# Kernel optimization log

Hardware: AMD Instinct MI355X
Metric: run time of the kernel (lower is better)

## Reference

```python
import jax, jax.numpy as jnp
import numpy as np

N = 100000
E = 600000
HID = 128
L = 2
BN_EPS = 1e-5


def setup_inputs() -> dict:
    key = jax.random.key(0)
    ks = jax.random.split(key, 20)
    s = 0.05
    inp = {
        "x": jax.random.normal(ks[0], (N, 128), jnp.float32),
        "edge_index": jax.random.randint(ks[1], (2, E), 0, N, jnp.int64 if jax.config.jax_enable_x64 else jnp.int32),
        "edge_attr": jax.random.normal(ks[2], (E, 1), jnp.float32),
        # backbone params
        "lin_W": jax.random.normal(ks[3], (128, HID), jnp.float32) * s,
        "lin_b": jnp.zeros((HID,), jnp.float32),
        "enc_W": jax.random.normal(ks[4], (1, HID), jnp.float32) * s,
        "enc_b": jnp.zeros((HID,), jnp.float32),
        # per-layer GIN params, stacked over L layers
        "eps": jnp.zeros((L,), jnp.float32),
        "e1_W": jax.random.normal(ks[5], (L, 1, HID), jnp.float32) * s,
        "e1_b": jnp.zeros((L, HID), jnp.float32),
        "e2_W": jax.random.normal(ks[6], (L, HID, HID), jnp.float32) * s,
        "e2_b": jnp.zeros((L, HID), jnp.float32),
        "m1_W": jax.random.normal(ks[7], (L, HID, 2 * HID), jnp.float32) * s,
        "m1_b": jnp.zeros((L, 2 * HID), jnp.float32),
        "bn_g": jnp.ones((L, 2 * HID), jnp.float32),
        "bn_b": jnp.zeros((L, 2 * HID), jnp.float32),
        "m2_W": jax.random.normal(ks[8], (L, 2 * HID, HID), jnp.float32) * s,
        "m2_b": jnp.zeros((L, HID), jnp.float32),
    }
    return inp


def _gin_layer(h, src, dst, edge_attr, eps, e1_W, e1_b, e2_W, e2_b,
               m1_W, m1_b, bn_g, bn_b, m2_W, m2_b):
    # edge encoder: Linear(1,H) -> ReLU -> Linear(H,H)
    ee = jax.nn.relu(edge_attr @ e1_W + e1_b) @ e2_W + e2_b      # [E,H]
    msg = jax.nn.relu(h[src] + ee)                               # gather + relu
    agg = jax.ops.segment_sum(msg, dst, num_segments=h.shape[0])  # scatter-add
    z = (1.0 + eps) * h + agg
    z = z @ m1_W + m1_b                                          # [N,2H]
    mu = jnp.mean(z, axis=0)
    var = jnp.mean((z - mu) ** 2, axis=0)                        # biased (train-mode BN)
    z = (z - mu) * jax.lax.rsqrt(var + BN_EPS) * bn_g + bn_b
    z = jax.nn.relu(z)
    return z @ m2_W + m2_b                                       # [N,H]


def reference(x, edge_index, edge_attr, lin_W, lin_b, enc_W, enc_b, eps,
              e1_W, e1_b, e2_W, e2_b, m1_W, m1_b, bn_g, bn_b, m2_W, m2_b):
    src, dst = edge_index[0], edge_index[1]
    # in_dim > 1 -> linear projection path
    h = x @ lin_W + lin_b                                        # [N,H]
    ee0 = edge_attr @ enc_W + enc_b                              # [E,H]
    new_h = h.at[src].set(jax.nn.relu(h[src] + ee0))
    new_h = new_h.at[dst].set(jax.nn.relu(h[dst] + ee0))
    h = new_h
    for l in range(L):
        h = _gin_layer(h, src, dst, edge_attr, eps[l], e1_W[l], e1_b[l],
                       e2_W[l], e2_b[l], m1_W[l], m1_b[l], bn_g[l], bn_b[l],
                       m2_W[l], m2_b[l])
        if l < L - 1:
            h = jax.nn.relu(h)
        # dropout omitted for determinism
    return h
```

## Files before the change

kernel.cpp:

```cpp
#include <hip/hip_runtime.h>

#define N_NODES 100000
#define E_EDGES 600000
#define HID 128

typedef __attribute__((ext_vector_type(8))) short short8v;
typedef __attribute__((ext_vector_type(4))) float f32x4;

__device__ __forceinline__ unsigned short bf16rne(float x) {
  unsigned u = __float_as_uint(x);
  return (unsigned short)((u + 0x7FFFu + ((u >> 16) & 1u)) >> 16);
}
__device__ __forceinline__ float bf16tof(unsigned short u) {
  return __uint_as_float(((unsigned)u) << 16);
}

__global__ void k_last(const int* __restrict__ ei, int* __restrict__ last_src,
                       int* __restrict__ last_dst, int* __restrict__ deg, int E) {
  int e = blockIdx.x * blockDim.x + threadIdx.x;
  if (e >= E) return;
  int s = ei[e], d = ei[E + e];
  atomicMax(&last_src[s], e);
  atomicMax(&last_dst[d], e);
  atomicAdd(&deg[d], 1);
}

__global__ __launch_bounds__(256) void k_scan1(const int* __restrict__ deg,
                                               int* __restrict__ excl,
                                               int* __restrict__ bsum, int n) {
  __shared__ int sh[256];
  int b = blockIdx.x, t = threadIdx.x;
  int i0 = b * 1024 + t * 4;
  int v0 = (i0 + 0 < n) ? deg[i0 + 0] : 0;
  int v1 = (i0 + 1 < n) ? deg[i0 + 1] : 0;
  int v2 = (i0 + 2 < n) ? deg[i0 + 2] : 0;
  int v3 = (i0 + 3 < n) ? deg[i0 + 3] : 0;
  int tsum = v0 + v1 + v2 + v3;
  sh[t] = tsum;
  __syncthreads();
  for (int off = 1; off < 256; off <<= 1) {
    int add = (t >= off) ? sh[t - off] : 0;
    __syncthreads();
    sh[t] += add;
    __syncthreads();
  }
  int ex = sh[t] - tsum;
  if (i0 + 0 < n) excl[i0 + 0] = ex;
  if (i0 + 1 < n) excl[i0 + 1] = ex + v0;
  if (i0 + 2 < n) excl[i0 + 2] = ex + v0 + v1;
  if (i0 + 3 < n) excl[i0 + 3] = ex + v0 + v1 + v2;
  if (t == 255) bsum[b] = sh[255];
}

__global__ void k_scan2(const int* __restrict__ bsum, int* __restrict__ boff, int nb) {
  __shared__ int sh[128];
  int t = threadIdx.x;
  int v = (t < nb) ? bsum[t] : 0;
  sh[t] = v;
  __syncthreads();
  for (int off = 1; off < 128; off <<= 1) {
    int add = (t >= off) ? sh[t - off] : 0;
    __syncthreads();
    sh[t] += add;
    __syncthreads();
  }
  if (t < nb) boff[t] = sh[t] - v;
}

__global__ void k_scatter(const int* __restrict__ ei, const float* __restrict__ ea,
                          const int* __restrict__ excl, const int* __restrict__ boff,
                          int* __restrict__ cnt, int2* __restrict__ pairE, int E) {
  int e = blockIdx.x * blockDim.x + threadIdx.x;
  if (e >= E) return;
  int d = ei[E + e];
  int p = excl[d] + boff[d >> 10] + atomicAdd(&cnt[d], 1);
  pairE[p] = make_int2(ei[e], __float_as_int(ea[e]));
}

__global__ void k_table(const float* __restrict__ e1_W, const float* __restrict__ e1_b,
                        const float* __restrict__ e2_W, const float* __restrict__ e2_b,
                        float* __restrict__ tabA, float* __restrict__ tabB,
                        float* __restrict__ tsort) {
  const int l = blockIdx.x;
  const float* W1g = e1_W + l * 128;
  const float* b1g = e1_b + l * 128;
  const float* W2g = e2_W + l * 128 * 128;
  const float* b2g = e2_b + l * 128;
  float* tA = tabA + (size_t)l * 129 * 128;
  float* tB = tabB + (size_t)l * 129 * 128;
  float* tS = tsort + l * 128;
  __shared__ float w1[128], b1[128], key[128];
  __shared__ int idx[128];
  __shared__ float w2[128][128];
  const int t = threadIdx.x;
  w1[t] = W1g[t];
  b1[t] = b1g[t];
  for (int k = 0; k < 128; ++k) w2[k][t] = W2g[k * 128 + t];
  __syncthreads();
  float s0 = w1[t];
  key[t] = (s0 != 0.0f) ? (-b1[t] / s0) : __builtin_inff();
  idx[t] = t;
  for (int size = 2; size <= 128; size <<= 1) {
    for (int stride = size >> 1; stride > 0; stride >>= 1) {
      __syncthreads();
      int p = t ^ stride;
      if (p > t) {
        bool up = ((t & size) == 0);
        float k1 = key[t], k2 = key[p];
        if (up == (k1 > k2)) {
          int i1 = idx[t], i2 = idx[p];
          key[t] = k2; key[p] = k1; idx[t] = i2; idx[p] = i1;
        }
      }
    }
  }
  __syncthreads();
  tS[t] = key[t];
  float A = 0.0f, B = b2g[t];
  for (int k = 0; k < 128; ++k) {
    float s = w1[k], bb = b1[k], w = w2[k][t];
    if (s < 0.0f) { A = fmaf(s, w, A); B = fmaf(bb, w, B); }
    else if (s == 0.0f && bb > 0.0f) { B = fmaf(bb, w, B); }
  }
  tA[t] = A;
  tB[t] = B;
  for (int i = 0; i < 128; ++i) {
    float kv = key[i];
    int kk = idx[i];
    if (kv < __builtin_inff()) {
      float s = w1[kk], bb = b1[kk], w = w2[kk][t];
      if (s > 0.0f) { A = fmaf(s, w, A); B = fmaf(bb, w, B); }
      else { A = fmaf(-s, w, A); B = fmaf(-bb, w, B); }
    }
    tA[(i + 1) * 128 + t] = A;
    tB[(i + 1) * 128 + t] = B;
  }
}

__global__ __launch_bounds__(256) void k_pos(const int2* __restrict__ pairE,
                                             const float* __restrict__ tsort,
                                             unsigned char* __restrict__ posb0,
                                             unsigned char* __restrict__ posb1, int E) {
  __shared__ float ts0[128], ts1[128];
  if (threadIdx.x < 128) {
    ts0[threadIdx.x] = tsort[threadIdx.x];
    ts1[threadIdx.x] = tsort[128 + threadIdx.x];
  }
  __syncthreads();
  int i = blockIdx.x * blockDim.x + threadIdx.x;
  if (i >= E) return;
  float a = __int_as_float(pairE[i].y);
  int p0 = 0, p1 = 0;
#pragma unroll
  for (int st = 64; st > 0; st >>= 1) {
    if (p0 + st <= 128 && ts0[p0 + st - 1] < a) p0 += st;
    if (p1 + st <= 128 && ts1[p1 + st - 1] < a) p1 += st;
  }
  posb0[i] = (unsigned char)p0;
  posb1[i] = (unsigned char)p1;
}

__global__ __launch_bounds__(256) void k_agg(
    const unsigned short* __restrict__ h, const int2* __restrict__ pairE,
    const unsigned char* __restrict__ posb, const int* __restrict__ excl,
    const int* __restrict__ boff, const float* __restrict__ tabA,
    const float* __restrict__ tabB, const float* __restrict__ epsP,
    unsigned* __restrict__ zin, int N, int E) {
  int w = __builtin_amdgcn_readfirstlane((int)((blockIdx.x * 256 + threadIdx.x) >> 6));
  if (w >= N) return;
  int lane = threadIdx.x & 63;
  int start = excl[w] + boff[w >> 10];
  int end = (w + 1 < N) ? (excl[w + 1] + boff[(w + 1) >> 10]) : E;
  int j = lane * 2;
  float a0 = 0.0f, a1 = 0.0f, c0 = 0.0f, c1 = 0.0f;
  int i = start;
  for (; i + 2 <= end; i += 2) {
    int2 pr0 = pairE[i], pr1 = pairE[i + 1];
    int p0 = posb[i], p1 = posb[i + 1];
    float aa = __int_as_float(pr0.y), ab = __int_as_float(pr1.y);
    unsigned hv0 = *(const unsigned*)(h + (size_t)pr0.x * HID + j);
    float2 A0 = *(const float2*)(tabA + (size_t)p0 * HID + j);
    float2 B0 = *(const float2*)(tabB + (size_t)p0 * HID + j);
    unsigned hv1 = *(const unsigned*)(h + (size_t)pr1.x * HID + j);
    float2 A1 = *(const float2*)(tabA + (size_t)p1 * HID + j);
    float2 B1 = *(const float2*)(tabB + (size_t)p1 * HID + j);
    a0 += fmaxf(__uint_as_float(hv0 << 16) + fmaf(A0.x, aa, B0.x), 0.0f);
    a1 += fmaxf(__uint_as_float(hv0 & 0xFFFF0000u) + fmaf(A0.y, aa, B0.y), 0.0f);
    c0 += fmaxf(__uint_as_float(hv1 << 16) + fmaf(A1.x, ab, B1.x), 0.0f);
    c1 += fmaxf(__uint_as_float(hv1 & 0xFFFF0000u) + fmaf(A1.y, ab, B1.y), 0.0f);
  }
  if (i < end) {
    int2 pr0 = pairE[i];
    int p0 = posb[i];
    float aa = __int_as_float(pr0.y);
    unsigned hv0 = *(const unsigned*)(h + (size_t)pr0.x * HID + j);
    float2 A0 = *(const float2*)(tabA + (size_t)p0 * HID + j);
    float2 B0 = *(const float2*)(tabB + (size_t)p0 * HID + j);
    a0 += fmaxf(__uint_as_float(hv0 << 16) + fmaf(A0.x, aa, B0.x), 0.0f);
    a1 += fmaxf(__uint_as_float(hv0 & 0xFFFF0000u) + fmaf(A0.y, aa, B0.y), 0.0f);
  }
  a0 += c0;
  a1 += c1;
  float ep1 = 1.0f + *epsP;
  unsigned hn = *(const unsigned*)(h + (size_t)w * HID + j);
  float ox = fmaf(ep1, __uint_as_float(hn << 16), a0);
  float oy = fmaf(ep1, __uint_as_float(hn & 0xFFFF0000u), a1);
  zin[(size_t)w * 64 + lane] = (unsigned)bf16rne(ox) | ((unsigned)bf16rne(oy) << 16);
}

__device__ __forceinline__ void pack_one(const float* __restrict__ W, int K, int M,
                                         int t, unsigned short* __restrict__ out) {
  int lane = t & 63, f = t >> 6;
  int KS = K >> 5;
  int mt = f / KS, ks = f - mt * KS;
  int col = mt * 16 + (lane & 15);
  int kb = ks * 32 + ((lane >> 4) * 8);
  unsigned r0, r1, r2, r3;
  r0 = bf16rne(W[(size_t)(kb + 0) * M + col]) | ((unsigned)bf16rne(W[(size_t)(kb + 1) * M + col]) << 16);
  r1 = bf16rne(W[(size_t)(kb + 2) * M + col]) | ((unsigned)bf16rne(W[(size_t)(kb + 3) * M + col]) << 16);
  r2 = bf16rne(W[(size_t)(kb + 4) * M + col]) | ((unsigned)bf16rne(W[(size_t)(kb + 5) * M + col]) << 16);
  r3 = bf16rne(W[(size_t)(kb + 6) * M + col]) | ((unsigned)bf16rne(W[(size_t)(kb + 7) * M + col]) << 16);
  uint4 v = make_uint4(r0, r1, r2, r3);
  *(uint4*)(out + ((size_t)f * 64 + lane) * 8) = v;
}

__global__ __launch_bounds__(256) void k_pack(
    const float* __restrict__ lin_W, const float* __restrict__ m1_W,
    const float* __restrict__ m2_W, unsigned short* __restrict__ pk_lin,
    unsigned short* __restrict__ pk_m1, unsigned short* __restrict__ pk_m2) {
  int t = blockIdx.x * 256 + threadIdx.x;
  if (t < 2048) {
    pack_one(lin_W, 128, 128, t, pk_lin);
  } else if (t < 10240) {
    int u = t - 2048;
    int l = u >> 12;
    pack_one(m1_W + (size_t)l * 128 * 256, 128, 256, u & 4095, pk_m1 + (size_t)l * 32768);
  } else if (t < 18432) {
    int u = t - 10240;
    int l = u >> 12;
    pack_one(m2_W + (size_t)l * 256 * 128, 256, 128, u & 4095, pk_m2 + (size_t)l * 32768);
  }
}

template <int K, int M, int MODE, bool RELU_OUT, bool OBF>
__global__ __launch_bounds__(256) void k_mgemm(
    const void* __restrict__ in0, const unsigned short* __restrict__ pkW,
    const float* __restrict__ bias, void* __restrict__ outv,
    const float* __restrict__ pre_a, const float* __restrict__ pre_b,
    float* __restrict__ pS1, float* __restrict__ pS2,
    const int* __restrict__ last_dst, const int* __restrict__ last_src,
    const float* __restrict__ ea, const float* __restrict__ encW,
    const float* __restrict__ encb) {
  constexpr int KS = K / 32, MT = M / 16;
  __shared__ float red[(MODE == 1) ? 2048 : 1];
  const int t = threadIdx.x;
  const int w = t >> 6, lane = t & 63;
  const int row0 = blockIdx.x * 64 + w * 16;
  const int arow = row0 + (lane & 15);
  const int rg = arow < N_NODES ? arow : N_NODES - 1;
  const int kb = (lane >> 4) * 8;

  short8v afrag[KS];
#pragma unroll
  for (int ks = 0; ks < KS; ++ks) {
    const int k0 = ks * 32 + kb;
    if (MODE == 0) {
      const float* in = (const float*)in0;
      float4 v0 = *(const float4*)(in + (size_t)rg * K + k0);
      float4 v1 = *(const float4*)(in + (size_t)rg * K + k0 + 4);
      short8v a;
      a[0] = (short)bf16rne(v0.x); a[1] = (short)bf16rne(v0.y);
      a[2] = (short)bf16rne(v0.z); a[3] = (short)bf16rne(v0.w);
      a[4] = (short)bf16rne(v1.x); a[5] = (short)bf16rne(v1.y);
      a[6] = (short)bf16rne(v1.z); a[7] = (short)bf16rne(v1.w);
      afrag[ks] = a;
    } else if (MODE == 1) {
      afrag[ks] = *(const short8v*)((const unsigned short*)in0 + (size_t)rg * K + k0);
    } else {
      short8v raw = *(const short8v*)((const unsigned short*)in0 + (size_t)rg * K + k0);
      float4 sa0 = *(const float4*)(pre_a + k0);
      float4 sa1 = *(const float4*)(pre_a + k0 + 4);
      float4 sb0 = *(const float4*)(pre_b + k0);
      float4 sb1 = *(const float4*)(pre_b + k0 + 4);
      short8v a;
      a[0] = (short)bf16rne(fmaxf(fmaf(bf16tof((unsigned short)raw[0]), sa0.x, sb0.x), 0.0f));
      a[1] = (short)bf16rne(fmaxf(fmaf(bf16tof((unsigned short)raw[1]), sa0.y, sb0.y), 0.0f));
      a[2] = (short)bf16rne(fmaxf(fmaf(bf16tof((unsigned short)raw[2]), sa0.z, sb0.z), 0.0f));
      a[3] = (short)bf16rne(fmaxf(fmaf(bf16tof((unsigned short)raw[3]), sa0.w, sb0.w), 0.0f));
      a[4] = (short)bf16rne(fmaxf(fmaf(bf16tof((unsigned short)raw[4]), sa1.x, sb1.x), 0.0f));
      a[5] = (short)bf16rne(fmaxf(fmaf(bf16tof((unsigned short)raw[5]), sa1.y, sb1.y), 0.0f));
      a[6] = (short)bf16rne(fmaxf(fmaf(bf16tof((unsigned short)raw[6]), sa1.z, sb1.z), 0.0f));
      a[7] = (short)bf16rne(fmaxf(fmaf(bf16tof((unsigned short)raw[7]), sa1.w, sb1.w), 0.0f));
      afrag[ks] = a;
    }
  }

  f32x4 acc[MT];
#pragma unroll
  for (int mt = 0; mt < MT; ++mt) acc[mt] = (f32x4){0.f, 0.f, 0.f, 0.f};
#pragma unroll
  for (int mt = 0; mt < MT; ++mt) {
#pragma unroll
    for (int ks = 0; ks < KS; ++ks) {
      short8v bfrag = *(const short8v*)(pkW + ((size_t)(mt * KS + ks) * 64 + lane) * 8);
      acc[mt] = __builtin_amdgcn_mfma_f32_16x16x32_bf16(afrag[ks], bfrag, acc[mt], 0, 0, 0);
    }
  }

  const int colb = lane & 15;
  const int rbase = row0 + (lane >> 4) * 4;
#pragma unroll
  for (int mt = 0; mt < MT; ++mt) {
    const int col = mt * 16 + colb;
    const float b = bias[col];
    if (MODE == 1) {
      unsigned short* out = (unsigned short*)outv;
      float s1 = 0.0f, s2 = 0.0f;
#pragma unroll
      for (int r = 0; r < 4; ++r) {
        int R = rbase + r;
        if (R < N_NODES) {
          float v = acc[mt][r] + b;
          out[(size_t)R * M + col] = bf16rne(v);
          s1 += v;
          s2 = fmaf(v, v, s2);
        }
      }
      s1 += __shfl_xor(s1, 16);
      s1 += __shfl_xor(s1, 32);
      s2 += __shfl_xor(s2, 16);
      s2 += __shfl_xor(s2, 32);
      if (lane < 16) {
        red[w * 256 + col] = s1;
        red[1024 + w * 256 + col] = s2;
      }
    } else if (MODE == 2) {
#pragma unroll
      for (int r = 0; r < 4; ++r) {
        int R = rbase + r;
        if (R < N_NODES) {
          float v = acc[mt][r] + b;
          if (RELU_OUT) v = fmaxf(v, 0.0f);
          if (OBF) ((unsigned short*)outv)[(size_t)R * M + col] = bf16rne(v);
          else ((float*)outv)[(size_t)R * M + col] = v;
        }
      }
    } else {
      const float ew = encW[col], eb = encb[col];
#pragma unroll
      for (int r = 0; r < 4; ++r) {
        int R = rbase + r;
        if (R < N_NODES) {
          float v = acc[mt][r] + b;
          int ld = last_dst[R];
          int ls = last_src[R];
          int e = (ld >= 0) ? ld : ls;
          if (e >= 0) v = fmaxf(v + fmaf(ea[e], ew, eb), 0.0f);
          ((unsigned short*)outv)[(size_t)R * M + col] = bf16rne(v);
        }
      }
    }
  }
  if (MODE == 1) {
    __syncthreads();
    if (t < 256) {
      float a = red[t] + red[256 + t] + red[512 + t] + red[768 + t];
      float q = red[1024 + t] + red[1280 + t] + red[1536 + t] + red[1792 + t];
      pS1[(size_t)blockIdx.x * 256 + t] = a;
      pS2[(size_t)blockIdx.x * 256 + t] = q;
    }
  }
}

__global__ __launch_bounds__(256) void k_bnred(
    const float* __restrict__ pS1, const float* __restrict__ pS2,
    float* __restrict__ qS1, float* __restrict__ qS2, int nblk) {
  int j = threadIdx.x;
  int b = blockIdx.x;
  float s1 = 0.0f, s2 = 0.0f;
  for (int i = b; i < nblk; i += 64) {
    s1 += pS1[(size_t)i * 256 + j];
    s2 += pS2[(size_t)i * 256 + j];
  }
  qS1[b * 256 + j] = s1;
  qS2[b * 256 + j] = s2;
}

__global__ __launch_bounds__(256) void k_bnfin2(
    const float* __restrict__ qS1, const float* __restrict__ qS2,
    const float* __restrict__ g, const float* __restrict__ bb,
    float* __restrict__ scale, float* __restrict__ shift) {
  int j = threadIdx.x;
  float s1 = 0.0f, s2 = 0.0f;
#pragma unroll 8
  for (int i = 0; i < 64; ++i) {
    s1 += qS1[i * 256 + j];
    s2 += qS2[i * 256 + j];
  }
  const float inv = 1.0f / (float)N_NODES;
  float mu = s1 * inv;
  float var = s2 * inv - mu * mu;
  float sc = g[j] * rsqrtf(var + 1e-5f);
  scale[j] = sc;
  shift[j] = fmaf(-mu, sc, bb[j]);
}

extern "C" void kernel_launch(void* const* d_in, const int* in_sizes, int n_in,
                              void* d_out, int out_size, void* d_ws, size_t ws_size,
                              hipStream_t stream) {
  const float* x     = (const float*)d_in[0];
  const int*   ei    = (const int*)d_in[1];
  const float* ea    = (const float*)d_in[2];
  const float* lin_W = (const float*)d_in[3];
  const float* lin_b = (const float*)d_in[4];
  const float* enc_W = (const float*)d_in[5];
  const float* enc_b = (const float*)d_in[6];
  const float* eps   = (const float*)d_in[7];
  const float* e1_W  = (const float*)d_in[8];
  const float* e1_b  = (const float*)d_in[9];
  const float* e2_W  = (const float*)d_in[10];
  const float* e2_b  = (const float*)d_in[11];
  const float* m1_W  = (const float*)d_in[12];
  const float* m1_b  = (const float*)d_in[13];
  const float* bn_g  = (const float*)d_in[14];
  const float* bn_b  = (const float*)d_in[15];
  const float* m2_W  = (const float*)d_in[16];
  const float* m2_b  = (const float*)d_in[17];

  const int NB_SCAN = (N_NODES + 1023) / 1024;
  const int NB_GEMM = (N_NODES + 63) / 64;

  float* ws = (float*)d_ws;
  size_t o = 0;
  unsigned short* hbuf = (unsigned short*)(ws + o); o += (size_t)N_NODES * 64;
  unsigned* zin_u = (unsigned*)(ws + o);            o += (size_t)N_NODES * 64;
  unsigned short* z2_u = (unsigned short*)(ws + o); o += (size_t)N_NODES * 128;
  int* last_dst = (int*)(ws + o);  o += N_NODES;
  int* last_src = (int*)(ws + o);  o += N_NODES;
  int* deg = (int*)(ws + o);       o += N_NODES;
  int* cnt = (int*)(ws + o);       o += N_NODES;
  int* excl = (int*)(ws + o);      o += N_NODES;
  int* bsum = (int*)(ws + o);      o += 128;
  int* boff = (int*)(ws + o);      o += 128;
  int2* pairE = (int2*)(ws + o);   o += (size_t)E_EDGES * 2;
  unsigned char* posb0 = (unsigned char*)(ws + o); o += (E_EDGES + 3) / 4 + 4;
  unsigned char* posb1 = (unsigned char*)(ws + o); o += (E_EDGES + 3) / 4 + 4;
  float* tabA = ws + o;            o += 2 * 129 * 128;
  float* tabB = ws + o;            o += 2 * 129 * 128;
  float* tsort = ws + o;           o += 2 * 128;
  float* pS1 = ws + o;             o += (size_t)NB_GEMM * 256;
  float* pS2 = ws + o;             o += (size_t)NB_GEMM * 256;
  float* qS1 = ws + o;             o += 64 * 256;
  float* qS2 = ws + o;             o += 64 * 256;
  float* scale = ws + o;           o += 256;
  float* shift = ws + o;           o += 256;
  unsigned short* pk_lin = (unsigned short*)(ws + o); o += 8192;
  unsigned short* pk_m1  = (unsigned short*)(ws + o); o += 32768;
  unsigned short* pk_m2  = (unsigned short*)(ws + o); o += 32768;
  if (ws_size < o * sizeof(float)) return;

  hipMemsetAsync(last_dst, 0xFF, 2 * (size_t)N_NODES * sizeof(int), stream);
  hipMemsetAsync(deg, 0, 2 * (size_t)N_NODES * sizeof(int), stream);
  k_table<<<2, 128, 0, stream>>>(e1_W, e1_b, e2_W, e2_b, tabA, tabB, tsort);
  k_last<<<(E_EDGES + 255) / 256, 256, 0, stream>>>(ei, last_src, last_dst, deg, E_EDGES);
  k_scan1<<<NB_SCAN, 256, 0, stream>>>(deg, excl, bsum, N_NODES);
  k_scan2<<<1, 128, 0, stream>>>(bsum, boff, NB_SCAN);
  k_scatter<<<(E_EDGES + 255) / 256, 256, 0, stream>>>(ei, ea, excl, boff, cnt, pairE, E_EDGES);
  k_pos<<<(E_EDGES + 255) / 256, 256, 0, stream>>>(pairE, tsort, posb0, posb1, E_EDGES);
  k_pack<<<72, 256, 0, stream>>>(lin_W, m1_W, m2_W, pk_lin, pk_m1, pk_m2);

  k_mgemm<128, 128, 0, false, true><<<NB_GEMM, 256, 0, stream>>>(
      x, pk_lin, lin_b, hbuf, nullptr, nullptr, nullptr, nullptr,
      last_dst, last_src, ea, enc_W, enc_b);

  for (int l = 0; l < 2; ++l) {
    k_agg<<<(N_NODES * 64 + 255) / 256, 256, 0, stream>>>(
        hbuf, pairE, l == 0 ? posb0 : posb1, excl, boff,
        tabA + (size_t)l * 129 * 128, tabB + (size_t)l * 129 * 128,
        eps + l, zin_u, N_NODES, E_EDGES);
    k_mgemm<128, 256, 1, false, true><<<NB_GEMM, 256, 0, stream>>>(
        zin_u, pk_m1 + (size_t)l * 32768, m1_b + l * 256, z2_u, nullptr, nullptr,
        pS1, pS2, nullptr, nullptr, nullptr, nullptr, nullptr);
    k_bnred<<<64, 256, 0, stream>>>(pS1, pS2, qS1, qS2, NB_GEMM);
    k_bnfin2<<<1, 256, 0, stream>>>(qS1, qS2, bn_g + l * 256, bn_b + l * 256,
                                    scale, shift);
    if (l == 0) {
      k_mgemm<256, 128, 2, true, true><<<NB_GEMM, 256, 0, stream>>>(
          z2_u, pk_m2, m2_b, hbuf, scale, shift,
          nullptr, nullptr, nullptr, nullptr, nullptr, nullptr, nullptr);
    } else {
      k_mgemm<256, 128, 2, false, false><<<NB_GEMM, 256, 0, stream>>>(
          z2_u, pk_m2 + 32768, m2_b + 128, d_out, scale, shift,
          nullptr, nullptr, nullptr, nullptr, nullptr, nullptr, nullptr);
    }
  }
}
```

Measured before the change: 642.6 us.

## Stage packed GEMM weights in LDS and pack per-node metadata into int4

Each GEMM block now copies the full packed bf16 weight matrix (up to 64KB) into shared memory before the MFMA loop, instead of having every wave read B fragments straight from global memory. Per-node last_src, last_dst, degree and counter arrays are merged into one int4 record, which is initialised by a small kernel instead of two memsets. The edge lookups in the projection epilogue are hoisted out of the column loop. The LDS staging adds a block-wide sync and a large shared-memory footprint that may reduce occupancy, and the int4 layout spreads atomics across wider records.

```diff
diff --git a/kernel.cpp b/kernel.cpp
--- a/kernel.cpp
+++ b/kernel.cpp
@@ -15,26 +15,30 @@
   return __uint_as_float(((unsigned)u) << 16);
 }
 
-__global__ void k_last(const int* __restrict__ ei, int* __restrict__ last_src,
-                       int* __restrict__ last_dst, int* __restrict__ deg, int E) {
+__global__ void k_init(int4* __restrict__ meta, int n) {
+  int i = blockIdx.x * blockDim.x + threadIdx.x;
+  if (i < n) meta[i] = make_int4(-1, -1, 0, 0);
+}
+
+__global__ void k_last(const int* __restrict__ ei, int4* __restrict__ meta, int E) {
   int e = blockIdx.x * blockDim.x + threadIdx.x;
   if (e >= E) return;
   int s = ei[e], d = ei[E + e];
-  atomicMax(&last_src[s], e);
-  atomicMax(&last_dst[d], e);
-  atomicAdd(&deg[d], 1);
-}
-
-__global__ __launch_bounds__(256) void k_scan1(const int* __restrict__ deg,
+  atomicMax(&meta[s].x, e);
+  atomicMax(&meta[d].y, e);
+  atomicAdd((unsigned*)&meta[d].z, 1u);
+}
+
+__global__ __launch_bounds__(256) void k_scan1(const int4* __restrict__ meta,
                                                int* __restrict__ excl,
                                                int* __restrict__ bsum, int n) {
   __shared__ int sh[256];
   int b = blockIdx.x, t = threadIdx.x;
   int i0 = b * 1024 + t * 4;
-  int v0 = (i0 + 0 < n) ? deg[i0 + 0] : 0;
-  int v1 = (i0 + 1 < n) ? deg[i0 + 1] : 0;
-  int v2 = (i0 + 2 < n) ? deg[i0 + 2] : 0;
-  int v3 = (i0 + 3 < n) ? deg[i0 + 3] : 0;
+  int v0 = (i0 + 0 < n) ? meta[i0 + 0].z : 0;
+  int v1 = (i0 + 1 < n) ? meta[i0 + 1].z : 0;
+  int v2 = (i0 + 2 < n) ? meta[i0 + 2].z : 0;
+  int v3 = (i0 + 3 < n) ? meta[i0 + 3].z : 0;
   int tsum = v0 + v1 + v2 + v3;
   sh[t] = tsum;
   __syncthreads();
@@ -69,11 +73,11 @@
 
 __global__ void k_scatter(const int* __restrict__ ei, const float* __restrict__ ea,
                           const int* __restrict__ excl, const int* __restrict__ boff,
-                          int* __restrict__ cnt, int2* __restrict__ pairE, int E) {
+                          int4* __restrict__ meta, int2* __restrict__ pairE, int E) {
   int e = blockIdx.x * blockDim.x + threadIdx.x;
   if (e >= E) return;
   int d = ei[E + e];
-  int p = excl[d] + boff[d >> 10] + atomicAdd(&cnt[d], 1);
+  int p = excl[d] + boff[d >> 10] + atomicAdd((unsigned*)&meta[d].w, 1u);
   pairE[p] = make_int2(ei[e], __float_as_int(ea[e]));
 }
 
@@ -248,10 +252,11 @@
     const float* __restrict__ bias, void* __restrict__ outv,
     const float* __restrict__ pre_a, const float* __restrict__ pre_b,
     float* __restrict__ pS1, float* __restrict__ pS2,
-    const int* __restrict__ last_dst, const int* __restrict__ last_src,
-    const float* __restrict__ ea, const float* __restrict__ encW,
-    const float* __restrict__ encb) {
+    const int4* __restrict__ meta, const float* __restrict__ ea,
+    const float* __restrict__ encW, const float* __restrict__ encb) {
   constexpr int KS = K / 32, MT = M / 16;
+  constexpr int NFRAG = MT * KS;
+  __shared__ unsigned short bsh[NFRAG * 512];
   __shared__ float red[(MODE == 1) ? 2048 : 1];
   const int t = threadIdx.x;
   const int w = t >> 6, lane = t & 63;
@@ -259,6 +264,16 @@
   const int arow = row0 + (lane & 15);
   const int rg = arow < N_NODES ? arow : N_NODES - 1;
   const int kb = (lane >> 4) * 8;
+
+  {
+    const uint4* gp = (const uint4*)pkW;
+    uint4* lp = (uint4*)bsh;
+#pragma unroll
+    for (int c = 0; c < NFRAG / 4; ++c) {
+      int idx = c * 256 + t;
+      lp[idx] = gp[idx];
+    }
+  }
 
   short8v afrag[KS];
 #pragma unroll
@@ -294,6 +309,7 @@
       afrag[ks] = a;
     }
   }
+  __syncthreads();
 
   f32x4 acc[MT];
 #pragma unroll
@@ -302,13 +318,25 @@
   for (int mt = 0; mt < MT; ++mt) {
 #pragma unroll
     for (int ks = 0; ks < KS; ++ks) {
-      short8v bfrag = *(const short8v*)(pkW + ((size_t)(mt * KS + ks) * 64 + lane) * 8);
+      short8v bfrag = *(const short8v*)&bsh[(mt * KS + ks) * 512 + lane * 8];
       acc[mt] = __builtin_amdgcn_mfma_f32_16x16x32_bf16(afrag[ks], bfrag, acc[mt], 0, 0, 0);
     }
   }
 
   const int colb = lane & 15;
   const int rbase = row0 + (lane >> 4) * 4;
+  int esel[4];
+  float eav[4];
+  if (MODE == 0) {
+#pragma unroll
+    for (int r = 0; r < 4; ++r) {
+      int R = rbase + r;
+      int4 m = (R < N_NODES) ? meta[R] : make_int4(-1, -1, 0, 0);
+      int e = (m.y >= 0) ? m.y : m.x;
+      esel[r] = e;
+      eav[r] = (e >= 0) ? ea[e] : 0.0f;
+    }
+  }
 #pragma unroll
   for (int mt = 0; mt < MT; ++mt) {
     const int col = mt * 16 + colb;
@@ -352,10 +380,7 @@
         int R = rbase + r;
         if (R < N_NODES) {
           float v = acc[mt][r] + b;
-          int ld = last_dst[R];
-          int ls = last_src[R];
-          int e = (ld >= 0) ? ld : ls;
-          if (e >= 0) v = fmaxf(v + fmaf(ea[e], ew, eb), 0.0f);
+          if (esel[r] >= 0) v = fmaxf(v + fmaf(eav[r], ew, eb), 0.0f);
           ((unsigned short*)outv)[(size_t)R * M + col] = bf16rne(v);
         }
       }
@@ -435,10 +460,7 @@
   unsigned short* hbuf = (unsigned short*)(ws + o); o += (size_t)N_NODES * 64;
   unsigned* zin_u = (unsigned*)(ws + o);            o += (size_t)N_NODES * 64;
   unsigned short* z2_u = (unsigned short*)(ws + o); o += (size_t)N_NODES * 128;
-  int* last_dst = (int*)(ws + o);  o += N_NODES;
-  int* last_src = (int*)(ws + o);  o += N_NODES;
-  int* deg = (int*)(ws + o);       o += N_NODES;
-  int* cnt = (int*)(ws + o);       o += N_NODES;
+  int4* meta = (int4*)(ws + o);    o += (size_t)N_NODES * 4;
   int* excl = (int*)(ws + o);      o += N_NODES;
   int* bsum = (int*)(ws + o);      o += 128;
   int* boff = (int*)(ws + o);      o += 128;
@@ -459,19 +481,18 @@
   unsigned short* pk_m2  = (unsigned short*)(ws + o); o += 32768;
   if (ws_size < o * sizeof(float)) return;
 
-  hipMemsetAsync(last_dst, 0xFF, 2 * (size_t)N_NODES * sizeof(int), stream);
-  hipMemsetAsync(deg, 0, 2 * (size_t)N_NODES * sizeof(int), stream);
+  k_init<<<(N_NODES + 255) / 256, 256, 0, stream>>>(meta, N_NODES);
   k_table<<<2, 128, 0, stream>>>(e1_W, e1_b, e2_W, e2_b, tabA, tabB, tsort);
-  k_last<<<(E_EDGES + 255) / 256, 256, 0, stream>>>(ei, last_src, last_dst, deg, E_EDGES);
-  k_scan1<<<NB_SCAN, 256, 0, stream>>>(deg, excl, bsum, N_NODES);
+  k_last<<<(E_EDGES + 255) / 256, 256, 0, stream>>>(ei, meta, E_EDGES);
+  k_scan1<<<NB_SCAN, 256, 0, stream>>>(meta, excl, bsum, N_NODES);
   k_scan2<<<1, 128, 0, stream>>>(bsum, boff, NB_SCAN);
-  k_scatter<<<(E_EDGES + 255) / 256, 256, 0, stream>>>(ei, ea, excl, boff, cnt, pairE, E_EDGES);
+  k_scatter<<<(E_EDGES + 255) / 256, 256, 0, stream>>>(ei, ea, excl, boff, meta, pairE, E_EDGES);
   k_pos<<<(E_EDGES + 255) / 256, 256, 0, stream>>>(pairE, tsort, posb0, posb1, E_EDGES);
   k_pack<<<72, 256, 0, stream>>>(lin_W, m1_W, m2_W, pk_lin, pk_m1, pk_m2);
 
   k_mgemm<128, 128, 0, false, true><<<NB_GEMM, 256, 0, stream>>>(
       x, pk_lin, lin_b, hbuf, nullptr, nullptr, nullptr, nullptr,
-      last_dst, last_src, ea, enc_W, enc_b);
+      meta, ea, enc_W, enc_b);
 
   for (int l = 0; l < 2; ++l) {
     k_agg<<<(N_NODES * 64 + 255) / 256, 256, 0, stream>>>(
@@ -480,18 +501,18 @@
         eps + l, zin_u, N_NODES, E_EDGES);
     k_mgemm<128, 256, 1, false, true><<<NB_GEMM, 256, 0, stream>>>(
         zin_u, pk_m1 + (size_t)l * 32768, m1_b + l * 256, z2_u, nullptr, nullptr,
-        pS1, pS2, nullptr, nullptr, nullptr, nullptr, nullptr);
+        pS1, pS2, nullptr, nullptr, nullptr, nullptr);
     k_bnred<<<64, 256, 0, stream>>>(pS1, pS2, qS1, qS2, NB_GEMM);
     k_bnfin2<<<1, 256, 0, stream>>>(qS1, qS2, bn_g + l * 256, bn_b + l * 256,
                                     scale, shift);
     if (l == 0) {
       k_mgemm<256, 128, 2, true, true><<<NB_GEMM, 256, 0, stream>>>(
           z2_u, pk_m2, m2_b, hbuf, scale, shift,
-          nullptr, nullptr, nullptr, nullptr, nullptr, nullptr, nullptr);
+          nullptr, nullptr, nullptr, nullptr, nullptr, nullptr);
     } else {
       k_mgemm<256, 128, 2, false, false><<<NB_GEMM, 256, 0, stream>>>(
           z2_u, pk_m2 + 32768, m2_b + 128, d_out, scale, shift,
-          nullptr, nullptr, nullptr, nullptr, nullptr, nullptr, nullptr);
-    }
-  }
-}
+          nullptr, nullptr, nullptr, nullptr, nullptr, nullptr);
+    }
+  }
+}
```

Result: no change. 630.2 us (-1.9%).
